# Optimization experiments

Measured on AMD Instinct MI355X. Metric: run time of the kernel, lower is better.

The kernel has to match this reference:

```python
import jax, jax.numpy as jnp
import numpy as np

ALPHA = 0.2  # leaky relu slope
NEG = -9e15  # mask fill value from pyGAT


def setup_inputs() -> dict:
    key = jax.random.key(0)
    ks = jax.random.split(key, 6)
    B, N, H, D = 1, 4096, 6, 1
    nheads, nhid, nclass = 8, 16, 1
    nfeat = H * D
    flow_x = jax.random.normal(ks[0], (B, N, H, D), dtype=jnp.float32)
    adj = jax.random.randint(ks[1], (N, N), 0, 2, dtype=jnp.int32)
    W = jax.random.normal(ks[2], (nheads, nfeat, nhid), dtype=jnp.float32) * 0.1
    a = jax.random.normal(ks[3], (nheads, 2 * nhid), dtype=jnp.float32) * 0.1
    W_out = jax.random.normal(ks[4], (nheads * nhid, nclass), dtype=jnp.float32) * 0.1
    a_out = jax.random.normal(ks[5], (2 * nclass,), dtype=jnp.float32) * 0.1
    return {"flow_x": flow_x, "adj": adj, "W": W, "a": a, "W_out": W_out, "a_out": a_out}


def reference(flow_x, adj, W, a, W_out, a_out):
    B, N, H, D = flow_x.shape
    x = flow_x.reshape(B, N, H * D)  # (B, N, nfeat)
    mask = adj > 0  # (N, N)

    # --- multi-head GAT layers (concat=True) ---
    O = W.shape[-1]
    Wh = jnp.einsum('bnf,hfo->bhno', x, W)  # (B, heads, N, O)
    e_src = jnp.einsum('bhno,ho->bhn', Wh, a[:, :O])
    e_dst = jnp.einsum('bhno,ho->bhn', Wh, a[:, O:])
    e = jax.nn.leaky_relu(e_src[..., :, None] + e_dst[..., None, :], ALPHA)  # (B, heads, N, N)
    att = jax.nn.softmax(jnp.where(mask, e, NEG), axis=-1)
    h = jax.nn.elu(jnp.einsum('bhnm,bhmo->bhno', att, Wh))  # (B, heads, N, O)
    x2 = jnp.transpose(h, (0, 2, 1, 3)).reshape(B, N, -1)  # head concat -> (B, N, heads*O)

    # --- output GAT layer (concat=False), then top-level ELU ---
    C = W_out.shape[-1]
    Wh2 = x2 @ W_out  # (B, N, C)
    e2 = jax.nn.leaky_relu((Wh2 @ a_out[:C])[:, :, None] + (Wh2 @ a_out[C:])[:, None, :], ALPHA)
    att2 = jax.nn.softmax(jnp.where(mask, e2, NEG), axis=-1)
    out = jax.nn.elu(jnp.einsum('bnm,bmc->bnc', att2, Wh2))  # (B, N, C)
    return out[:, :, None, :]  # (B, N, 1, C)
```

## Files before the change

kernel.cpp:

```cpp
#include <hip/hip_runtime.h>
#include <stdint.h>

#define N 4096
#define NF 6
#define NO 16

typedef _Float16 half8 __attribute__((ext_vector_type(8)));
typedef float floatx4 __attribute__((ext_vector_type(4)));

#define OFF_WHF  0
#define OFF_ES   1048576
#define OFF_EN   1179648
#define OFF_EN2  1310720
#define OFF_ED   1441792
#define OFF_F    1572864
#define OFF_F2   1703936
#define OFF_X2   1835008
#define OFF_WH2  3932160
#define OFF_ED2  3948544
#define OFF_BITS 3964928

__global__ __launch_bounds__(256) void k_wh(const float* __restrict__ x,
                                            const float* __restrict__ W,
                                            const float* __restrict__ a,
                                            _Float16* __restrict__ Whf,
                                            float* __restrict__ es,
                                            float* __restrict__ en,
                                            float* __restrict__ en2,
                                            float* __restrict__ ed,
                                            float* __restrict__ fq,
                                            float* __restrict__ fq2) {
    int tid = blockIdx.x * 256 + threadIdx.x;
    int n = tid >> 3, h = tid & 7;
    float xf[NF];
#pragma unroll
    for (int f = 0; f < NF; ++f) xf[f] = x[n * NF + f];
    float wh[NO];
#pragma unroll
    for (int o = 0; o < NO; ++o) {
        float s = 0.f;
#pragma unroll
        for (int f = 0; f < NF; ++f) s = fmaf(xf[f], W[(h * NF + f) * NO + o], s);
        wh[o] = s;
    }
    float s1 = 0.f, s2 = 0.f;
#pragma unroll
    for (int o = 0; o < NO; ++o) {
        s1 = fmaf(wh[o], a[h * 32 + o], s1);
        s2 = fmaf(wh[o], a[h * 32 + 16 + o], s2);
    }
    int tile = n >> 5, q = (n >> 3) & 3, j = n & 7;
    _Float16* base = Whf + ((size_t)((h << 7) + tile) << 9) + j;
#pragma unroll
    for (int o = 0; o < NO; ++o) base[(size_t)(((q << 4) + o) << 3)] = (_Float16)wh[o];
    int idx = (h << 12) + n;
    es[idx]  = s1;
    en[idx]  = __expf(s1);
    en2[idx] = __expf(0.2f * s1);
    ed[idx]  = s2;
    fq[idx]  = __expf(s2);
    fq2[idx] = __expf(0.2f * s2);
}

__global__ __launch_bounds__(256) void k_bits(const int* __restrict__ adj,
                                              unsigned long long* __restrict__ bits) {
    int lane = threadIdx.x & 63;
    int wv = threadIdx.x >> 6;
    int n = blockIdx.x;
    int wbase = wv << 4;
    const int* row = adj + (size_t)n * N + (wbase << 6) + lane;
    int v[16];
#pragma unroll
    for (int i = 0; i < 16; ++i) v[i] = row[i << 6];
    unsigned long long b[16];
#pragma unroll
    for (int i = 0; i < 16; ++i) b[i] = __ballot(v[i] != 0);
    if (lane == 0) {
#pragma unroll
        for (int i = 0; i < 16; ++i)
            bits[((size_t)(wbase + i) << 12) + n] = b[i];
    }
}

__global__ __launch_bounds__(256, 4) void k_attn1(const _Float16* __restrict__ Whf,
                                                  const float* __restrict__ es,
                                                  const float* __restrict__ en,
                                                  const float* __restrict__ en2,
                                                  const float* __restrict__ ed,
                                                  const float* __restrict__ fq,
                                                  const float* __restrict__ fq2,
                                                  const uint32_t* __restrict__ bits,
                                                  float* __restrict__ x2) {
    int h = blockIdx.x >> 7;
    int rg = blockIdx.x & 127;
    int lane = threadIdx.x & 63;
    int wv = threadIdx.x >> 6;
    int l15 = lane & 15, q = lane >> 4, qb = q << 3;
    int rowb = rg << 5;

    __shared__ float red[32][17];
    for (int i = threadIdx.x; i < 32 * 17; i += 256) ((float*)red)[i] = 0.f;
    __syncthreads();

    float esn[2], Ena[2], Enb[2];
    int rowoff[2];
#pragma unroll
    for (int t = 0; t < 2; ++t) {
        int row = rowb + (t << 4) + l15;
        esn[t] = es[(h << 12) + row];
        Ena[t] = en[(h << 12) + row];
        Enb[t] = en2[(h << 12) + row];
        rowoff[t] = row << 1;
    }

    floatx4 acc[2], accd[2];
#pragma unroll
    for (int t = 0; t < 2; ++t)
#pragma unroll
        for (int r = 0; r < 4; ++r) { acc[t][r] = 0.f; accd[t][r] = 0.f; }

    half8 ones;
#pragma unroll
    for (int j = 0; j < 8; ++j) ones[j] = (_Float16)1.0f;

    const float* edh = ed  + (h << 12);
    const float* Fh  = fq  + (h << 12);
    const float* F2h = fq2 + (h << 12);

    for (int step = 0; step < 32; ++step) {
        int m0 = (wv << 10) + (step << 5);
        const floatx4* pe = (const floatx4*)(edh + m0 + qb);
        const floatx4* pf = (const floatx4*)(Fh  + m0 + qb);
        const floatx4* pg = (const floatx4*)(F2h + m0 + qb);
        floatx4 ea = pe[0], eb = pe[1];
        floatx4 fa = pf[0], fb = pf[1];
        floatx4 ga = pg[0], gb = pg[1];
        float edj[8] = {ea[0],ea[1],ea[2],ea[3],eb[0],eb[1],eb[2],eb[3]};
        float Fj [8] = {fa[0],fa[1],fa[2],fa[3],fb[0],fb[1],fb[2],fb[3]};
        float F2j[8] = {ga[0],ga[1],ga[2],ga[3],gb[0],gb[1],gb[2],gb[3]};
        half8 bfrag = *(const half8*)(Whf + ((size_t)((h << 7) + (m0 >> 5)) << 9) + (lane << 3));
        int wbase = ((m0 >> 6) << 13) + ((m0 >> 5) & 1);
#pragma unroll
        for (int t = 0; t < 2; ++t) {
            uint32_t w = bits[wbase + rowoff[t]] >> qb;
            half8 afrag;
#pragma unroll
            for (int j = 0; j < 8; ++j) {
                float s = esn[t] + edj[j];
                bool pos = (s >= 0.f);
                float ff = pos ? Fj[j]  : F2j[j];
                float gg = pos ? Ena[t] : Enb[t];
                float e = ff * gg;
                e = (w & (1u << j)) ? e : 0.f;
                afrag[j] = (_Float16)e;
            }
            acc[t]  = __builtin_amdgcn_mfma_f32_16x16x32_f16(afrag, bfrag, acc[t], 0, 0, 0);
            accd[t] = __builtin_amdgcn_mfma_f32_16x16x32_f16(afrag, ones,  accd[t], 0, 0, 0);
        }
    }

#pragma unroll
    for (int t = 0; t < 2; ++t)
#pragma unroll
        for (int r = 0; r < 4; ++r)
            atomicAdd(&red[(t << 4) + (q << 2) + r][l15], acc[t][r]);
    if (l15 == 0) {
#pragma unroll
        for (int t = 0; t < 2; ++t)
#pragma unroll
            for (int r = 0; r < 4; ++r)
                atomicAdd(&red[(t << 4) + (q << 2) + r][16], accd[t][r]);
    }
    __syncthreads();

#pragma unroll
    for (int i = threadIdx.x; i < 512; i += 256) {
        int r2 = i >> 4, c2 = i & 15;
        float v = red[r2][c2] / red[r2][16];
        v = v > 0.f ? v : expm1f(v);
        x2[(size_t)(rowb + r2) * 128 + (h << 4) + c2] = v;
    }
}

__global__ __launch_bounds__(256) void k_wh2(const float* __restrict__ x2,
                                             const float* __restrict__ W_out,
                                             const float* __restrict__ a_out,
                                             float* __restrict__ Wh2,
                                             float* __restrict__ ed2) {
    int lane = threadIdx.x & 63;
    int n = (blockIdx.x << 2) + (threadIdx.x >> 6);
    const float2* xp = (const float2*)(x2 + (size_t)n * 128);
    const float2* wp = (const float2*)W_out;
    float2 xv = xp[lane], wv2 = wp[lane];
    float s = fmaf(xv.x, wv2.x, xv.y * wv2.y);
#pragma unroll
    for (int off = 32; off; off >>= 1) s += __shfl_xor(s, off);
    if (lane == 0) { Wh2[n] = s; ed2[n] = s * a_out[1]; }
}

__global__ __launch_bounds__(256) void k_attn2(const float* __restrict__ Wh2,
                                               const float* __restrict__ ed2,
                                               const float* __restrict__ a_out,
                                               const unsigned long long* __restrict__ bits,
                                               float* __restrict__ out) {
    int n = blockIdx.x;
    int lane = threadIdx.x & 63;
    int wv = threadIdx.x >> 6;
    float esn = Wh2[n] * a_out[0];
    float num = 0.f, den = 0.f;
#pragma unroll
    for (int it = 0; it < 16; ++it) {
        int w = (wv << 4) + it;
        int m = (w << 6) + lane;
        float w2 = Wh2[m];
        float s = esn + ed2[m];
        unsigned long long wb = bits[((size_t)w << 12) + n];
        s = fmaxf(s, 0.2f * s);
        float e = __expf(s);
        e = ((wb >> lane) & 1ull) ? e : 0.f;
        num = fmaf(e, w2, num);
        den += e;
    }
#pragma unroll
    for (int off = 32; off; off >>= 1) {
        num += __shfl_xor(num, off);
        den += __shfl_xor(den, off);
    }
    __shared__ float rn[4], rd[4];
    if (lane == 0) { rn[wv] = num; rd[wv] = den; }
    __syncthreads();
    if (threadIdx.x == 0) {
        float nn = rn[0] + rn[1] + rn[2] + rn[3];
        float dd = rd[0] + rd[1] + rd[2] + rd[3];
        float v = nn / dd;
        out[n] = v > 0.f ? v : expm1f(v);
    }
}

extern "C" void kernel_launch(void* const* d_in, const int* in_sizes, int n_in,
                              void* d_out, int out_size, void* d_ws, size_t ws_size,
                              hipStream_t stream) {
    const float* x     = (const float*)d_in[0];
    const int*   adj   = (const int*)d_in[1];
    const float* W     = (const float*)d_in[2];
    const float* a     = (const float*)d_in[3];
    const float* W_out = (const float*)d_in[4];
    const float* a_out = (const float*)d_in[5];
    float* out = (float*)d_out;

    char* ws = (char*)d_ws;
    _Float16* Whf = (_Float16*)(ws + OFF_WHF);
    float* es  = (float*)(ws + OFF_ES);
    float* en  = (float*)(ws + OFF_EN);
    float* en2 = (float*)(ws + OFF_EN2);
    float* ed  = (float*)(ws + OFF_ED);
    float* fq  = (float*)(ws + OFF_F);
    float* fq2 = (float*)(ws + OFF_F2);
    float* x2  = (float*)(ws + OFF_X2);
    float* Wh2 = (float*)(ws + OFF_WH2);
    float* ed2 = (float*)(ws + OFF_ED2);
    unsigned long long* bits = (unsigned long long*)(ws + OFF_BITS);

    hipLaunchKernelGGL(k_wh,    dim3(128),  dim3(256), 0, stream,
                       x, W, a, Whf, es, en, en2, ed, fq, fq2);
    hipLaunchKernelGGL(k_bits,  dim3(4096), dim3(256), 0, stream, adj, bits);
    hipLaunchKernelGGL(k_attn1, dim3(1024), dim3(256), 0, stream,
                       Whf, es, en, en2, ed, fq, fq2, (const uint32_t*)bits, x2);
    hipLaunchKernelGGL(k_wh2,   dim3(1024), dim3(256), 0, stream, x2, W_out, a_out, Wh2, ed2);
    hipLaunchKernelGGL(k_attn2, dim3(4096), dim3(256), 0, stream, Wh2, ed2, a_out, bits, out);
}
```

Measured before the change: 179.7 us.

## Replace leaky-relu branch with max of exponentials and halve rows per block

Because exp is monotonic, exp(leaky_relu(s)) equals the maximum of exp(s) and exp(0.2*s), so the attention weight becomes max(En*F, En2*F2). This drops the es/ed arrays, their loads and the per-element add/compare/select. Each k_attn1 block now handles 16 rows instead of 32, which doubles the grid to 2048 blocks. The trade-off is that the Whf, F and F2 loads are reused across only one row tile, so each column fragment is fetched twice as often.

```diff
diff --git a/kernel.cpp b/kernel.cpp
--- a/kernel.cpp
+++ b/kernel.cpp
@@ -9,25 +9,21 @@
 typedef float floatx4 __attribute__((ext_vector_type(4)));
 
 #define OFF_WHF  0
-#define OFF_ES   1048576
-#define OFF_EN   1179648
-#define OFF_EN2  1310720
-#define OFF_ED   1441792
-#define OFF_F    1572864
-#define OFF_F2   1703936
-#define OFF_X2   1835008
-#define OFF_WH2  3932160
-#define OFF_ED2  3948544
-#define OFF_BITS 3964928
+#define OFF_EN   1048576
+#define OFF_EN2  1179648
+#define OFF_F    1310720
+#define OFF_F2   1441792
+#define OFF_X2   1572864
+#define OFF_WH2  3670016
+#define OFF_ED2  3686400
+#define OFF_BITS 3702784
 
 __global__ __launch_bounds__(256) void k_wh(const float* __restrict__ x,
                                             const float* __restrict__ W,
                                             const float* __restrict__ a,
                                             _Float16* __restrict__ Whf,
-                                            float* __restrict__ es,
                                             float* __restrict__ en,
                                             float* __restrict__ en2,
-                                            float* __restrict__ ed,
                                             float* __restrict__ fq,
                                             float* __restrict__ fq2) {
     int tid = blockIdx.x * 256 + threadIdx.x;
@@ -54,10 +50,8 @@
 #pragma unroll
     for (int o = 0; o < NO; ++o) base[(size_t)(((q << 4) + o) << 3)] = (_Float16)wh[o];
     int idx = (h << 12) + n;
-    es[idx]  = s1;
     en[idx]  = __expf(s1);
     en2[idx] = __expf(0.2f * s1);
-    ed[idx]  = s2;
     fq[idx]  = __expf(s2);
     fq2[idx] = __expf(0.2f * s2);
 }
@@ -83,99 +77,72 @@
 }
 
 __global__ __launch_bounds__(256, 4) void k_attn1(const _Float16* __restrict__ Whf,
-                                                  const float* __restrict__ es,
                                                   const float* __restrict__ en,
                                                   const float* __restrict__ en2,
-                                                  const float* __restrict__ ed,
                                                   const float* __restrict__ fq,
                                                   const float* __restrict__ fq2,
                                                   const uint32_t* __restrict__ bits,
                                                   float* __restrict__ x2) {
-    int h = blockIdx.x >> 7;
-    int rg = blockIdx.x & 127;
+    int h = blockIdx.x >> 8;
+    int rg = blockIdx.x & 255;
     int lane = threadIdx.x & 63;
     int wv = threadIdx.x >> 6;
     int l15 = lane & 15, q = lane >> 4, qb = q << 3;
-    int rowb = rg << 5;
-
-    __shared__ float red[32][17];
-    for (int i = threadIdx.x; i < 32 * 17; i += 256) ((float*)red)[i] = 0.f;
+    int rowb = rg << 4;
+
+    __shared__ float red[16][17];
+    for (int i = threadIdx.x; i < 16 * 17; i += 256) ((float*)red)[i] = 0.f;
     __syncthreads();
 
-    float esn[2], Ena[2], Enb[2];
-    int rowoff[2];
-#pragma unroll
-    for (int t = 0; t < 2; ++t) {
-        int row = rowb + (t << 4) + l15;
-        esn[t] = es[(h << 12) + row];
-        Ena[t] = en[(h << 12) + row];
-        Enb[t] = en2[(h << 12) + row];
-        rowoff[t] = row << 1;
-    }
-
-    floatx4 acc[2], accd[2];
-#pragma unroll
-    for (int t = 0; t < 2; ++t)
-#pragma unroll
-        for (int r = 0; r < 4; ++r) { acc[t][r] = 0.f; accd[t][r] = 0.f; }
+    int row = rowb + l15;
+    float Ena = en [(h << 12) + row];
+    float Enb = en2[(h << 12) + row];
+    int rowoff = row << 1;
+
+    floatx4 acc, accd;
+#pragma unroll
+    for (int r = 0; r < 4; ++r) { acc[r] = 0.f; accd[r] = 0.f; }
 
     half8 ones;
 #pragma unroll
     for (int j = 0; j < 8; ++j) ones[j] = (_Float16)1.0f;
 
-    const float* edh = ed  + (h << 12);
     const float* Fh  = fq  + (h << 12);
     const float* F2h = fq2 + (h << 12);
 
     for (int step = 0; step < 32; ++step) {
         int m0 = (wv << 10) + (step << 5);
-        const floatx4* pe = (const floatx4*)(edh + m0 + qb);
         const floatx4* pf = (const floatx4*)(Fh  + m0 + qb);
         const floatx4* pg = (const floatx4*)(F2h + m0 + qb);
-        floatx4 ea = pe[0], eb = pe[1];
         floatx4 fa = pf[0], fb = pf[1];
         floatx4 ga = pg[0], gb = pg[1];
-        float edj[8] = {ea[0],ea[1],ea[2],ea[3],eb[0],eb[1],eb[2],eb[3]};
         float Fj [8] = {fa[0],fa[1],fa[2],fa[3],fb[0],fb[1],fb[2],fb[3]};
         float F2j[8] = {ga[0],ga[1],ga[2],ga[3],gb[0],gb[1],gb[2],gb[3]};
         half8 bfrag = *(const half8*)(Whf + ((size_t)((h << 7) + (m0 >> 5)) << 9) + (lane << 3));
-        int wbase = ((m0 >> 6) << 13) + ((m0 >> 5) & 1);
-#pragma unroll
-        for (int t = 0; t < 2; ++t) {
-            uint32_t w = bits[wbase + rowoff[t]] >> qb;
-            half8 afrag;
-#pragma unroll
-            for (int j = 0; j < 8; ++j) {
-                float s = esn[t] + edj[j];
-                bool pos = (s >= 0.f);
-                float ff = pos ? Fj[j]  : F2j[j];
-                float gg = pos ? Ena[t] : Enb[t];
-                float e = ff * gg;
-                e = (w & (1u << j)) ? e : 0.f;
-                afrag[j] = (_Float16)e;
-            }
-            acc[t]  = __builtin_amdgcn_mfma_f32_16x16x32_f16(afrag, bfrag, acc[t], 0, 0, 0);
-            accd[t] = __builtin_amdgcn_mfma_f32_16x16x32_f16(afrag, ones,  accd[t], 0, 0, 0);
+        uint32_t w = bits[((m0 >> 6) << 13) + ((m0 >> 5) & 1) + rowoff] >> qb;
+        half8 afrag;
+#pragma unroll
+        for (int j = 0; j < 8; ++j) {
+            float e = fmaxf(Ena * Fj[j], Enb * F2j[j]);
+            e = (w & (1u << j)) ? e : 0.f;
+            afrag[j] = (_Float16)e;
         }
-    }
-
-#pragma unroll
-    for (int t = 0; t < 2; ++t)
+        acc  = __builtin_amdgcn_mfma_f32_16x16x32_f16(afrag, bfrag, acc,  0, 0, 0);
+        accd = __builtin_amdgcn_mfma_f32_16x16x32_f16(afrag, ones,  accd, 0, 0, 0);
+    }
+
+#pragma unroll
+    for (int r = 0; r < 4; ++r)
+        atomicAdd(&red[(q << 2) + r][l15], acc[r]);
+    if (l15 == 0) {
 #pragma unroll
         for (int r = 0; r < 4; ++r)
-            atomicAdd(&red[(t << 4) + (q << 2) + r][l15], acc[t][r]);
-    if (l15 == 0) {
-#pragma unroll
-        for (int t = 0; t < 2; ++t)
-#pragma unroll
-            for (int r = 0; r < 4; ++r)
-                atomicAdd(&red[(t << 4) + (q << 2) + r][16], accd[t][r]);
+            atomicAdd(&red[(q << 2) + r][16], accd[r]);
     }
     __syncthreads();
 
-#pragma unroll
-    for (int i = threadIdx.x; i < 512; i += 256) {
-        int r2 = i >> 4, c2 = i & 15;
+    {
+        int r2 = threadIdx.x >> 4, c2 = threadIdx.x & 15;
         float v = red[r2][c2] / red[r2][16];
         v = v > 0.f ? v : expm1f(v);
         x2[(size_t)(rowb + r2) * 128 + (h << 4) + c2] = v;
@@ -250,10 +217,8 @@
 
     char* ws = (char*)d_ws;
     _Float16* Whf = (_Float16*)(ws + OFF_WHF);
-    float* es  = (float*)(ws + OFF_ES);
     float* en  = (float*)(ws + OFF_EN);
     float* en2 = (float*)(ws + OFF_EN2);
-    float* ed  = (float*)(ws + OFF_ED);
     float* fq  = (float*)(ws + OFF_F);
     float* fq2 = (float*)(ws + OFF_F2);
     float* x2  = (float*)(ws + OFF_X2);
@@ -262,10 +227,10 @@
     unsigned long long* bits = (unsigned long long*)(ws + OFF_BITS);
 
     hipLaunchKernelGGL(k_wh,    dim3(128),  dim3(256), 0, stream,
-                       x, W, a, Whf, es, en, en2, ed, fq, fq2);
+                       x, W, a, Whf, en, en2, fq, fq2);
     hipLaunchKernelGGL(k_bits,  dim3(4096), dim3(256), 0, stream, adj, bits);
-    hipLaunchKernelGGL(k_attn1, dim3(1024), dim3(256), 0, stream,
-                       Whf, es, en, en2, ed, fq, fq2, (const uint32_t*)bits, x2);
+    hipLaunchKernelGGL(k_attn1, dim3(2048), dim3(256), 0, stream,
+                       Whf, en, en2, fq, fq2, (const uint32_t*)bits, x2);
     hipLaunchKernelGGL(k_wh2,   dim3(1024), dim3(256), 0, stream, x2, W_out, a_out, Wh2, ed2);
     hipLaunchKernelGGL(k_attn2, dim3(4096), dim3(256), 0, stream, Wh2, ed2, a_out, bits, out);
 }
```

Measured after the change: 176.7 us. Within noise of the previous version (-1.7%).
